# Kernel tuning notes

Hardware: AMD Instinct MI355X
Metric: run time of the kernel (lower is better)

Reference implementation:

```python
import jax, jax.numpy as jnp
import numpy as np

B, EMBED, HIDDEN, NH, D, H, W = 8, 384, 512, 32, 12, 32, 32  # attn_size D = EMBED // NH
SCALE = float(D) ** -0.5


def conv1x1(x, Wm, b):
    # 1x1 conv == per-pixel linear: x (B,Cin,H,W), Wm (Cout,Cin), b (Cout,)
    return jnp.einsum('bchw,oc->bohw', x, Wm) + b[None, :, None, None]


def mha(qc, kc, vc):
    # qc/kc/vc: (B, EMBED, H, W); tokens = H*W, heads = NH, head_dim = D
    HW = H * W
    def split(t):
        return t.reshape(B, NH, D, HW).transpose(0, 1, 3, 2)  # (B, nh, HW, d)
    q = split(qc) * SCALE
    k = split(kc)
    v = split(vc)
    w = jax.nn.softmax(jnp.einsum('bhnd,bhmd->bhnm', q, k), axis=-1)  # (B,nh,HW,HW)
    f = jnp.einsum('bhnm,bhmd->bhnd', w, v)  # (B,nh,HW,d)
    # (B,nh,HW,d) -> (B,HW,nh,d) -> (B,H,W,C) -> (B,C,H,W), matching torch view
    return f.transpose(0, 2, 1, 3).reshape(B, H, W, NH * D).transpose(0, 3, 1, 2)


def setup_inputs() -> dict:
    key = jax.random.key(0)
    ks = jax.random.split(key, 18)
    def p(k, shape):
        return jax.random.normal(k, shape, dtype=jnp.float32) * 0.02
    return {
        'x': jax.random.normal(ks[0], (B, EMBED, H, W), dtype=jnp.float32),
        'x_bpf': jax.random.normal(ks[1], (B, EMBED, H, W), dtype=jnp.float32),
        'Wq': p(ks[2], (EMBED, EMBED)), 'bq': p(ks[3], (EMBED,)),
        'Wk': p(ks[4], (EMBED, EMBED)), 'bk': p(ks[5], (EMBED,)),
        'Wv': p(ks[6], (EMBED, EMBED)), 'bv': p(ks[7], (EMBED,)),
        'Wq_bpf': p(ks[8], (EMBED, EMBED)), 'bq_bpf': p(ks[9], (EMBED,)),
        'Wk_bpf': p(ks[10], (EMBED, EMBED)), 'bk_bpf': p(ks[11], (EMBED,)),
        'Wv_bpf': p(ks[12], (EMBED, EMBED)), 'bv_bpf': p(ks[13], (EMBED,)),
        'Wo': p(ks[14], (HIDDEN, 2 * EMBED)), 'bo': p(ks[15], (HIDDEN,)),
    }


def reference(x, x_bpf, Wq, bq, Wk, bk, Wv, bv, Wq_bpf, bq_bpf, Wk_bpf, bk_bpf, Wv_bpf, bv_bpf, Wo, bo):
    q = conv1x1(x, Wq, bq)
    k = conv1x1(x, Wk, bk)
    v = conv1x1(x, Wv, bv)
    q_bpf = conv1x1(x_bpf, Wq_bpf, bq_bpf)
    k_bpf = conv1x1(x_bpf, Wk_bpf, bk_bpf)
    v_bpf = conv1x1(x_bpf, Wv_bpf, bv_bpf)
    # branch 1: query from bpf stream, key/value from x stream, residual to x
    f = mha(q_bpf, k, v) + x
    # branch 2: query from x stream, key/value from bpf stream, residual to x_bpf
    f_bpf = mha(q, k_bpf, v_bpf) + x_bpf
    fused = jnp.concatenate([f, f_bpf], axis=1)  # (B, 2*EMBED, H, W)
    return conv1x1(fused, Wo, bo)  # (B, HIDDEN, H, W)
```

## Files before the change

### kernel.cpp

```cpp
#include <hip/hip_runtime.h>
#include <hip/hip_bf16.h>

#define BB 8
#define EMBED 384
#define NH 32
#define HD 12
#define HWN 1024
#define HIDDEN 512
#define KTOT 1536
#define SCALE 0.28867513459481287f

typedef __attribute__((ext_vector_type(8))) unsigned short ushort8;
typedef __attribute__((ext_vector_type(8))) short short8;
typedef __attribute__((ext_vector_type(4))) float f32x4;
typedef __attribute__((ext_vector_type(16))) float f32x16;
typedef __attribute__((ext_vector_type(4))) unsigned short ushort4v;
typedef __attribute__((ext_vector_type(2))) unsigned int uint2v;

static __device__ __forceinline__ float bf2f(unsigned short u) {
    return __uint_as_float(((unsigned int)u) << 16);
}
static __device__ __forceinline__ unsigned short f2bf(float f) {
    unsigned int u = __float_as_uint(f);
    u = u + 0x7FFFu + ((u >> 16) & 1u);
    return (unsigned short)(u >> 16);
}
static __device__ __forceinline__ unsigned int cvt_pk_bf16(float lo, float hi) {
    unsigned int r;
    asm("v_cvt_pk_bf16_f32 %0, %1, %2" : "=v"(r) : "v"(lo), "v"(hi));
    return r;
}

#if __has_builtin(__builtin_amdgcn_global_load_lds)
#define HAVE_GLOAD_LDS 1
static __device__ __forceinline__ void gl_lds16(const unsigned short* g, unsigned short* l) {
    __builtin_amdgcn_global_load_lds(
        (const __attribute__((address_space(1))) unsigned int*)g,
        (__attribute__((address_space(3))) unsigned int*)l, 16, 0, 0);
}
#else
#define HAVE_GLOAD_LDS 0
#endif

struct WConv {
    const float* src[7];
    unsigned short* dst[7];
    int start[8];
};

__global__ __launch_bounds__(256) void k_bf16_all(WConv wc) {
    int i = blockIdx.x * 256 + threadIdx.x;
    if (i >= wc.start[7]) return;
    int p = 0;
#pragma unroll
    for (int j = 1; j < 7; ++j) p += (i >= wc.start[j]);
    const int e = i - wc.start[p];
    const f32x4 v = reinterpret_cast<const f32x4*>(wc.src[p])[e];
    ushort4v o;
#pragma unroll
    for (int j = 0; j < 4; ++j) o[j] = f2bf(v[j]);
    if (p == 6) {
        const int row = e / 192, cc = e % 192;
        ushort4v* d = reinterpret_cast<ushort4v*>(wc.dst[6]);
        d[row * 384 + cc] = o;
        d[row * 384 + 192 + cc] = o;
    } else {
        reinterpret_cast<ushort4v*>(wc.dst[p])[e] = o;
    }
}

__global__ __launch_bounds__(256) void k_transpose(const float* __restrict__ x0, const float* __restrict__ x1,
                                                   unsigned short* __restrict__ fused2) {
    __shared__ float tile[32][33];
    const int z = blockIdx.z;
    const int s = z >> 3, b = z & 7;
    const float* src = (s ? x1 : x0) + (size_t)b * EMBED * HWN;
    unsigned short* dst = fused2 + (size_t)b * HWN * KTOT + 768 + s * 384;
    const int c0 = blockIdx.x * 32;
    const int n0 = blockIdx.y * 32;
    const int tc = threadIdx.x & 31;
    const int tr = threadIdx.x >> 5;
#pragma unroll
    for (int p = 0; p < 4; ++p) {
        int r = tr + p * 8;
        tile[r][tc] = src[(size_t)(c0 + r) * HWN + n0 + tc];
    }
    __syncthreads();
#pragma unroll
    for (int p = 0; p < 4; ++p) {
        int r = tr + p * 8;
        dst[(size_t)(n0 + r) * KTOT + c0 + tc] = f2bf(tile[tc][r]);
    }
}

template <bool F32OUT>
static __device__ __forceinline__ void gemm128(const unsigned short* __restrict__ A, int lda,
                                               const unsigned short* __restrict__ Bt, int ldb,
                                               const float* __restrict__ bias,
                                               unsigned short* __restrict__ outBf,
                                               float* __restrict__ outF,
                                               int K, int bx, int by) {
    __shared__ unsigned short As[128][64];
    __shared__ unsigned short Bs[128][64];
    const int t = threadIdx.x;
    const int lane = t & 63;
    const int w = t >> 6;
    const int wr = w >> 1, wc = w & 1;
    const int o0 = bx * 128, n0 = by * 128;
    const int srow = lane >> 3;
    const int scol = (((lane & 7) ^ (lane >> 3)) << 3);

    f32x4 acc[4][4] = {};

    for (int k0 = 0; k0 < K; k0 += 64) {
#pragma unroll
        for (int i = 0; i < 4; ++i) {
            const int c = w * 4 + i;
            const int r = c * 8 + srow;
#if HAVE_GLOAD_LDS
            gl_lds16(A + (size_t)(o0 + r) * lda + k0 + scol, &As[c * 8][0]);
            gl_lds16(Bt + (size_t)(n0 + r) * ldb + k0 + scol, &Bs[c * 8][0]);
#else
            *reinterpret_cast<ushort8*>(&As[r][(lane & 7) * 8]) =
                *reinterpret_cast<const ushort8*>(A + (size_t)(o0 + r) * lda + k0 + scol);
            *reinterpret_cast<ushort8*>(&Bs[r][(lane & 7) * 8]) =
                *reinterpret_cast<const ushort8*>(Bt + (size_t)(n0 + r) * ldb + k0 + scol);
#endif
        }
        __syncthreads();
#pragma unroll
        for (int kk = 0; kk < 2; ++kk) {
            const int ko = kk * 32 + ((lane >> 4) << 3);
            const int xorb = (lane & 7) << 4;
            short8 af[4], bf[4];
#pragma unroll
            for (int i = 0; i < 4; ++i) {
                const int ra = wr * 64 + i * 16 + (lane & 15);
                const int rb = wc * 64 + i * 16 + (lane & 15);
                af[i] = *reinterpret_cast<const short8*>(
                    reinterpret_cast<const char*>(&As[0][0]) + ra * 128 + ((ko * 2) ^ xorb));
                bf[i] = *reinterpret_cast<const short8*>(
                    reinterpret_cast<const char*>(&Bs[0][0]) + rb * 128 + ((ko * 2) ^ xorb));
            }
#pragma unroll
            for (int i = 0; i < 4; ++i)
#pragma unroll
                for (int j = 0; j < 4; ++j)
                    acc[i][j] = __builtin_amdgcn_mfma_f32_16x16x32_bf16(af[i], bf[j], acc[i][j], 0, 0, 0);
        }
        __syncthreads();
    }
#pragma unroll
    for (int i = 0; i < 4; ++i) {
#pragma unroll
        for (int j = 0; j < 4; ++j) {
            const int ob = o0 + wr * 64 + i * 16 + ((lane >> 4) << 2);
            const int n  = n0 + wc * 64 + j * 16 + (lane & 15);
#pragma unroll
            for (int r = 0; r < 4; ++r) {
                const int o = ob + r;
                float v = acc[i][j][r] + bias[o];
                if constexpr (F32OUT) outF[(size_t)o * HWN + n] = v;
                else                  outBf[(size_t)o * HWN + n] = f2bf(v);
            }
        }
    }
}

struct QkvTable {
    const unsigned short* W[6];
    const float* bias[6];
    const unsigned short* fused2;
    unsigned short* out[6];
};

__global__ __launch_bounds__(256) void k_gemm_qkv(QkvTable tab) {
    const int bid = blockIdx.x;
    const int xcd = bid & 7;
    const int slot = bid >> 3;
    const int bx = slot % 3;
    const int g = (slot / 3) * 8 + xcd;
    const int by = g & 7;
    const int z = g >> 3;
    const int b = z / 6, p = z % 6;
    const unsigned short* Bt = tab.fused2 + (size_t)b * HWN * KTOT + 768 + (p / 3) * 384;
    gemm128<false>(tab.W[p], EMBED, Bt, KTOT, tab.bias[p],
                   tab.out[p] + (size_t)b * EMBED * HWN, nullptr,
                   EMBED, bx, by);
}

__global__ __launch_bounds__(256) void k_gemm_out(const unsigned short* __restrict__ Wo2,
                                                  const unsigned short* __restrict__ fused2,
                                                  const float* __restrict__ bo,
                                                  float* __restrict__ out) {
    const int bid = blockIdx.x;
    const int xcd = bid & 7;
    const int slot = bid >> 3;
    const int bx = slot & 3;
    const int g = ((slot >> 2) << 3) | xcd;
    const int by = g & 7;
    const int b = g >> 3;
    gemm128<true>(Wo2, KTOT, fused2 + (size_t)b * HWN * KTOT, KTOT, bo,
                  nullptr, out + (size_t)b * HIDDEN * HWN,
                  KTOT, bx, by);
}

#define OT_STRIDE 416
__global__ __launch_bounds__(512) void k_attn_mfma(const unsigned short* __restrict__ qc,
                                                   const unsigned short* __restrict__ kc,
                                                   const unsigned short* __restrict__ vc,
                                                   const unsigned short* __restrict__ qcb,
                                                   const unsigned short* __restrict__ kcb,
                                                   const unsigned short* __restrict__ vcb,
                                                   unsigned short* __restrict__ fused2) {
    __shared__ unsigned short Ks[256][18];
    __shared__ unsigned short Vs[13][264];

    const int bid = blockIdx.x;
    const int inst = bid & 511, qt = bid >> 9;
    const int branch = inst >> 8, b = (inst >> 5) & 7, h = inst & 31;
    const unsigned short* Qg = branch ? qc : qcb;
    const unsigned short* Kg = branch ? kcb : kc;
    const unsigned short* Vg = branch ? vcb : vc;
    const int coff = branch ? 384 : 0;
    const size_t base = ((size_t)b * EMBED + h * HD) * HWN;
    const int t = threadIdx.x;
    const int lane = t & 63, w = t >> 6;
    const int q31 = lane & 31, hi = lane >> 5;
    const int n0 = qt * 256;
    const float C2 = SCALE * 1.4426950408889634f;

    short8 qf = {};
    {
        const int qg = n0 + w * 32 + q31;
#pragma unroll
        for (int j = 0; j < 8; ++j) {
            const int d = hi * 8 + j;
            if (d < HD)
                qf[j] = (short)f2bf(bf2f(Qg[base + (size_t)d * HWN + qg]) * C2);
        }
    }

    f32x16 acc, z16;
#pragma unroll
    for (int r = 0; r < 16; ++r) { acc[r] = 0.f; z16[r] = 0.f; }
    const int vrow = (q31 < HD) ? q31 : 12;

    for (int phase = 0; phase < 4; ++phase) {
        const int m0 = phase << 8;
        __syncthreads();
        if (w < 6) {
            const size_t kb = base + (size_t)(2 * w) * HWN + m0;
#pragma unroll
            for (int it = 0; it < 4; ++it) {
                const int m = it * 64 + lane;
                const unsigned int da = (unsigned int)Kg[kb + m] | ((unsigned int)Kg[kb + HWN + m] << 16);
                *reinterpret_cast<unsigned int*>(&Ks[m][2 * w]) = da;
            }
        } else {
            const int cz = 12 + 2 * (w - 6);
#pragma unroll
            for (int it = 0; it < 4; ++it) {
                const int m = it * 64 + lane;
                *reinterpret_cast<unsigned int*>(&Ks[m][cz]) = 0u;
            }
        }
        if (w < 6) {
            const int d = 2 * w + (lane >> 5);
            const int col = (lane & 31) * 8;
            *reinterpret_cast<ushort8*>(&Vs[d][col]) =
                *reinterpret_cast<const ushort8*>(&Vg[base + (size_t)d * HWN + m0 + col]);
        } else if (w == 6 && lane < 32) {
            ushort8 ones;
#pragma unroll
            for (int j = 0; j < 8; ++j) ones[j] = 0x3F80;
            *reinterpret_cast<ushort8*>(&Vs[12][lane * 8]) = ones;
        }
        __syncthreads();

        __builtin_amdgcn_s_setprio(1);
        for (int mc = 0; mc < 8; ++mc) {
            const int mb = mc << 5;
            union { short8 v; unsigned int u[4]; } kf;
            {
                const unsigned int* kp = reinterpret_cast<const unsigned int*>(&Ks[mb + q31][hi * 8]);
                kf.u[0] = kp[0]; kf.u[1] = kp[1]; kf.u[2] = kp[2]; kf.u[3] = kp[3];
            }
            union { short8 v; uint2v u2[2]; } vf1, vf2;
            vf1.u2[0] = *reinterpret_cast<const uint2v*>(&Vs[vrow][mb + hi * 4]);
            vf1.u2[1] = *reinterpret_cast<const uint2v*>(&Vs[vrow][mb + 8 + hi * 4]);
            vf2.u2[0] = *reinterpret_cast<const uint2v*>(&Vs[vrow][mb + 16 + hi * 4]);
            vf2.u2[1] = *reinterpret_cast<const uint2v*>(&Vs[vrow][mb + 24 + hi * 4]);
            const f32x16 s = __builtin_amdgcn_mfma_f32_32x32x16_bf16(kf.v, qf, z16, 0, 0, 0);
            union { short8 v; unsigned int u[4]; } p1, p2;
#pragma unroll
            for (int r = 0; r < 4; ++r) {
                p1.u[r] = cvt_pk_bf16(__builtin_amdgcn_exp2f(s[2 * r]),
                                      __builtin_amdgcn_exp2f(s[2 * r + 1]));
                p2.u[r] = cvt_pk_bf16(__builtin_amdgcn_exp2f(s[8 + 2 * r]),
                                      __builtin_amdgcn_exp2f(s[8 + 2 * r + 1]));
            }
            acc = __builtin_amdgcn_mfma_f32_32x32x16_bf16(p1.v, vf1.v, acc, 0, 0, 0);
            acc = __builtin_amdgcn_mfma_f32_32x32x16_bf16(p2.v, vf2.v, acc, 0, 0, 0);
        }
        __builtin_amdgcn_s_setprio(0);
    }

    float invq[16];
#pragma unroll
    for (int r = 0; r < 16; ++r)
        invq[r] = 1.0f / __shfl(acc[r], (lane & 32) | 12);

    __syncthreads();
    {
        unsigned short* OtW = &Ks[0][0] + w * OT_STRIDE;
        if (q31 < HD) {
#pragma unroll
            for (int r2 = 0; r2 < 8; ++r2) {
                const int r = 2 * r2;
                const int q = (r & 3) + 8 * (r >> 2) + 4 * hi;
                const unsigned int dw = (unsigned int)f2bf(acc[r] * invq[r]) |
                                        ((unsigned int)f2bf(acc[r + 1] * invq[r + 1]) << 16);
                *reinterpret_cast<unsigned int*>(&OtW[q31 * 32 + q]) = dw;
            }
        }
    }
    __syncthreads();
    {
        const int q = t >> 1, half = t & 1;
        const unsigned short* Osrc = &Ks[0][0] + (q >> 5) * OT_STRIDE + (half * 6) * 32 + (q & 31);
        unsigned int dwv[3];
#pragma unroll
        for (int dp = 0; dp < 3; ++dp)
            dwv[dp] = (unsigned int)Osrc[(2 * dp) * 32] | ((unsigned int)Osrc[(2 * dp + 1) * 32] << 16);
        unsigned int* dst = reinterpret_cast<unsigned int*>(
            fused2 + ((size_t)b * HWN + n0 + q) * KTOT + coff + h * HD + half * 6);
#pragma unroll
        for (int dp = 0; dp < 3; ++dp) dst[dp] = dwv[dp];
    }
}

extern "C" void kernel_launch(void* const* d_in, const int* in_sizes, int n_in,
                              void* d_out, int out_size, void* d_ws, size_t ws_size,
                              hipStream_t stream) {
    (void)in_sizes; (void)n_in; (void)out_size; (void)ws_size;
    const float* x   = (const float*)d_in[0];
    const float* xbp = (const float*)d_in[1];
    const float* Wq  = (const float*)d_in[2];  const float* bq  = (const float*)d_in[3];
    const float* Wk  = (const float*)d_in[4];  const float* bk  = (const float*)d_in[5];
    const float* Wv  = (const float*)d_in[6];  const float* bv  = (const float*)d_in[7];
    const float* Wqb = (const float*)d_in[8];  const float* bqb = (const float*)d_in[9];
    const float* Wkb = (const float*)d_in[10]; const float* bkb = (const float*)d_in[11];
    const float* Wvb = (const float*)d_in[12]; const float* bvb = (const float*)d_in[13];
    const float* Wo  = (const float*)d_in[14]; const float* bo  = (const float*)d_in[15];
    float* out = (float*)d_out;

    char* ws = (char*)d_ws;
    size_t off = 0;
    auto alloc = [&](size_t bytes) -> void* {
        void* p = ws + off;
        off = (off + bytes + 255) & ~(size_t)255;
        return p;
    };
    unsigned short* wbf[6];
    for (int i = 0; i < 6; ++i) wbf[i] = (unsigned short*)alloc((size_t)EMBED * EMBED * 2);
    unsigned short* wo2 = (unsigned short*)alloc((size_t)HIDDEN * KTOT * 2);
    unsigned short* qkv[6];
    for (int i = 0; i < 6; ++i) qkv[i] = (unsigned short*)alloc((size_t)BB * EMBED * HWN * 2);
    unsigned short* fused2 = (unsigned short*)alloc((size_t)BB * HWN * KTOT * 2);

    WConv wc;
    const float* wsrc[7] = {Wq, Wk, Wv, Wqb, Wkb, Wvb, Wo};
    unsigned short* wdst[7] = {wbf[0], wbf[1], wbf[2], wbf[3], wbf[4], wbf[5], wo2};
    int acc4 = 0;
    for (int i = 0; i < 7; ++i) {
        const int n = (i < 6) ? EMBED * EMBED : HIDDEN * 768;
        wc.src[i] = wsrc[i];
        wc.dst[i] = wdst[i];
        wc.start[i] = acc4;
        acc4 += n / 4;
    }
    wc.start[7] = acc4;
    k_bf16_all<<<(acc4 + 255) / 256, 256, 0, stream>>>(wc);

    k_transpose<<<dim3(EMBED / 32, HWN / 32, 16), 256, 0, stream>>>(x, xbp, fused2);

    QkvTable tab;
    tab.W[0] = wbf[0]; tab.W[1] = wbf[1]; tab.W[2] = wbf[2];
    tab.W[3] = wbf[3]; tab.W[4] = wbf[4]; tab.W[5] = wbf[5];
    tab.bias[0] = bq; tab.bias[1] = bk; tab.bias[2] = bv;
    tab.bias[3] = bqb; tab.bias[4] = bkb; tab.bias[5] = bvb;
    tab.fused2 = fused2;
    for (int i = 0; i < 6; ++i) tab.out[i] = qkv[i];
    k_gemm_qkv<<<dim3(1152), 256, 0, stream>>>(tab);

    k_attn_mfma<<<dim3(2048), 512, 0, stream>>>(qkv[0], qkv[1], qkv[2], qkv[3], qkv[4], qkv[5],
                                                fused2);

    k_gemm_out<<<dim3(256), 256, 0, stream>>>(wo2, fused2, bo, out);
}
```

Measured before the change: 140.2 us.

## Double-buffer K/V LDS tiles in attention kernel with register prefetch

The attention kernel now keeps two LDS buffers for the K and V tiles. The next phase's K/V data is loaded into registers before the current phase's MFMA loop and written to the alternate buffer afterwards, so each phase needs one barrier instead of two. The constant zero-padding columns and the ones row are written once up front instead of every phase. This aims to hide global-load latency behind compute, at the cost of roughly doubling shared memory for these tiles and adding register pressure, which may reduce occupancy.

```diff
diff --git a/kernel.cpp b/kernel.cpp
--- a/kernel.cpp
+++ b/kernel.cpp
@@ -213,8 +213,8 @@
                                                    const unsigned short* __restrict__ kcb,
                                                    const unsigned short* __restrict__ vcb,
                                                    unsigned short* __restrict__ fused2) {
-    __shared__ unsigned short Ks[256][18];
-    __shared__ unsigned short Vs[13][264];
+    __shared__ unsigned short Ks[2][256][18];
+    __shared__ unsigned short Vs[2][13][264];
 
     const int bid = blockIdx.x;
     const int inst = bid & 511, qt = bid >> 9;
@@ -241,56 +241,75 @@
         }
     }
 
+    if (w >= 6) {
+        const int cz = 12 + 2 * (w - 6);
+#pragma unroll
+        for (int buf = 0; buf < 2; ++buf)
+#pragma unroll
+            for (int it = 0; it < 4; ++it) {
+                const int m = it * 64 + lane;
+                *reinterpret_cast<unsigned int*>(&Ks[buf][m][cz]) = 0u;
+            }
+    }
+    if (w == 6 && lane < 32) {
+        ushort8 ones;
+#pragma unroll
+        for (int j = 0; j < 8; ++j) ones[j] = 0x3F80;
+        *reinterpret_cast<ushort8*>(&Vs[0][12][lane * 8]) = ones;
+        *reinterpret_cast<ushort8*>(&Vs[1][12][lane * 8]) = ones;
+    }
+
     f32x16 acc, z16;
 #pragma unroll
     for (int r = 0; r < 16; ++r) { acc[r] = 0.f; z16[r] = 0.f; }
     const int vrow = (q31 < HD) ? q31 : 12;
 
+    unsigned short kr0, kr1, kr2, kr3, kr4, kr5, kr6, kr7;
+    ushort8 vreg = {};
+
+    auto LOADS = [&](int phase) {
+        if (w < 6) {
+            const int m0 = phase << 8;
+            const size_t kb = base + (size_t)(2 * w) * HWN + m0;
+            kr0 = Kg[kb + lane];           kr1 = Kg[kb + HWN + lane];
+            kr2 = Kg[kb + 64 + lane];      kr3 = Kg[kb + HWN + 64 + lane];
+            kr4 = Kg[kb + 128 + lane];     kr5 = Kg[kb + HWN + 128 + lane];
+            kr6 = Kg[kb + 192 + lane];     kr7 = Kg[kb + HWN + 192 + lane];
+            const int d = 2 * w + (lane >> 5);
+            vreg = *reinterpret_cast<const ushort8*>(&Vg[base + (size_t)d * HWN + m0 + (lane & 31) * 8]);
+        }
+    };
+    auto WRITES = [&](int buf) {
+        if (w < 6) {
+            *reinterpret_cast<unsigned int*>(&Ks[buf][lane][2 * w])       = (unsigned int)kr0 | ((unsigned int)kr1 << 16);
+            *reinterpret_cast<unsigned int*>(&Ks[buf][64 + lane][2 * w])  = (unsigned int)kr2 | ((unsigned int)kr3 << 16);
+            *reinterpret_cast<unsigned int*>(&Ks[buf][128 + lane][2 * w]) = (unsigned int)kr4 | ((unsigned int)kr5 << 16);
+            *reinterpret_cast<unsigned int*>(&Ks[buf][192 + lane][2 * w]) = (unsigned int)kr6 | ((unsigned int)kr7 << 16);
+            const int d = 2 * w + (lane >> 5);
+            *reinterpret_cast<ushort8*>(&Vs[buf][d][(lane & 31) * 8]) = vreg;
+        }
+    };
+
+    LOADS(0);
+    WRITES(0);
     for (int phase = 0; phase < 4; ++phase) {
-        const int m0 = phase << 8;
+        if (phase < 3) LOADS(phase + 1);
         __syncthreads();
-        if (w < 6) {
-            const size_t kb = base + (size_t)(2 * w) * HWN + m0;
-#pragma unroll
-            for (int it = 0; it < 4; ++it) {
-                const int m = it * 64 + lane;
-                const unsigned int da = (unsigned int)Kg[kb + m] | ((unsigned int)Kg[kb + HWN + m] << 16);
-                *reinterpret_cast<unsigned int*>(&Ks[m][2 * w]) = da;
-            }
-        } else {
-            const int cz = 12 + 2 * (w - 6);
-#pragma unroll
-            for (int it = 0; it < 4; ++it) {
-                const int m = it * 64 + lane;
-                *reinterpret_cast<unsigned int*>(&Ks[m][cz]) = 0u;
-            }
-        }
-        if (w < 6) {
-            const int d = 2 * w + (lane >> 5);
-            const int col = (lane & 31) * 8;
-            *reinterpret_cast<ushort8*>(&Vs[d][col]) =
-                *reinterpret_cast<const ushort8*>(&Vg[base + (size_t)d * HWN + m0 + col]);
-        } else if (w == 6 && lane < 32) {
-            ushort8 ones;
-#pragma unroll
-            for (int j = 0; j < 8; ++j) ones[j] = 0x3F80;
-            *reinterpret_cast<ushort8*>(&Vs[12][lane * 8]) = ones;
-        }
-        __syncthreads();
+        const int buf = phase & 1;
 
         __builtin_amdgcn_s_setprio(1);
         for (int mc = 0; mc < 8; ++mc) {
             const int mb = mc << 5;
             union { short8 v; unsigned int u[4]; } kf;
             {
-                const unsigned int* kp = reinterpret_cast<const unsigned int*>(&Ks[mb + q31][hi * 8]);
+                const unsigned int* kp = reinterpret_cast<const unsigned int*>(&Ks[buf][mb + q31][hi * 8]);
                 kf.u[0] = kp[0]; kf.u[1] = kp[1]; kf.u[2] = kp[2]; kf.u[3] = kp[3];
             }
             union { short8 v; uint2v u2[2]; } vf1, vf2;
-            vf1.u2[0] = *reinterpret_cast<const uint2v*>(&Vs[vrow][mb + hi * 4]);
-            vf1.u2[1] = *reinterpret_cast<const uint2v*>(&Vs[vrow][mb + 8 + hi * 4]);
-            vf2.u2[0] = *reinterpret_cast<const uint2v*>(&Vs[vrow][mb + 16 + hi * 4]);
-            vf2.u2[1] = *reinterpret_cast<const uint2v*>(&Vs[vrow][mb + 24 + hi * 4]);
+            vf1.u2[0] = *reinterpret_cast<const uint2v*>(&Vs[buf][vrow][mb + hi * 4]);
+            vf1.u2[1] = *reinterpret_cast<const uint2v*>(&Vs[buf][vrow][mb + 8 + hi * 4]);
+            vf2.u2[0] = *reinterpret_cast<const uint2v*>(&Vs[buf][vrow][mb + 16 + hi * 4]);
+            vf2.u2[1] = *reinterpret_cast<const uint2v*>(&Vs[buf][vrow][mb + 24 + hi * 4]);
             const f32x16 s = __builtin_amdgcn_mfma_f32_32x32x16_bf16(kf.v, qf, z16, 0, 0, 0);
             union { short8 v; unsigned int u[4]; } p1, p2;
 #pragma unroll
@@ -304,6 +323,8 @@
             acc = __builtin_amdgcn_mfma_f32_32x32x16_bf16(p2.v, vf2.v, acc, 0, 0, 0);
         }
         __builtin_amdgcn_s_setprio(0);
+
+        if (phase < 3) WRITES((phase + 1) & 1);
     }
 
     float invq[16];
@@ -313,7 +334,7 @@
 
     __syncthreads();
     {
-        unsigned short* OtW = &Ks[0][0] + w * OT_STRIDE;
+        unsigned short* OtW = &Ks[0][0][0] + w * OT_STRIDE;
         if (q31 < HD) {
 #pragma unroll
             for (int r2 = 0; r2 < 8; ++r2) {
@@ -328,7 +349,7 @@
     __syncthreads();
     {
         const int q = t >> 1, half = t & 1;
-        const unsigned short* Osrc = &Ks[0][0] + (q >> 5) * OT_STRIDE + (half * 6) * 32 + (q & 31);
+        const unsigned short* Osrc = &Ks[0][0][0] + (q >> 5) * OT_STRIDE + (half * 6) * 32 + (q & 31);
         unsigned int dwv[3];
 #pragma unroll
         for (int dp = 0; dp < 3; ++dp)
```

Measured after the change: 136.8 us. 2.4% less time.
